# Kernel optimization log

Hardware: AMD Instinct MI355X
Metric: run time of the kernel (lower is better)

The kernel has to match this reference:

```python
import math
import jax, jax.numpy as jnp
import numpy as np

B, S, D, H = 2, 2048, 2048, 16
HD = D // H
SCALE = 1.0 / math.sqrt(HD)


def setup_inputs() -> dict:
    key = jax.random.key(0)
    kx, kq, kk, kv, ko = jax.random.split(key, 5)
    w_std = 1.0 / math.sqrt(D)
    return {
        "x": jax.random.normal(kx, (B, S, D), jnp.float32),
        "Wq": jax.random.normal(kq, (D, D), jnp.float32) * w_std,
        "Wk": jax.random.normal(kk, (D, D), jnp.float32) * w_std,
        "Wv": jax.random.normal(kv, (D, D), jnp.float32) * w_std,
        "Wo": jax.random.normal(ko, (D, D), jnp.float32) * w_std,
        "attention_mask": jnp.ones((B, S), jnp.int32),
        "sliding_window": 512,
        "sink_tokens": 4,
    }


def reference(x, Wq, Wk, Wv, Wo, attention_mask, sliding_window, sink_tokens):
    b, s, d = x.shape
    # nn.Linear(bias=False): y = x @ W^T
    q = (x @ Wq.T).reshape(b, s, H, HD).transpose(0, 2, 1, 3)  # [b,h,s,hd]
    k = (x @ Wk.T).reshape(b, s, H, HD).transpose(0, 2, 1, 3)
    v = (x @ Wv.T).reshape(b, s, H, HD).transpose(0, 2, 1, 3)

    scores = jnp.einsum("bhqd,bhkd->bhqk", q, k) * SCALE  # [b,h,s,s]

    i = jnp.arange(s)[:, None]
    j = jnp.arange(s)[None, :]
    causal = j <= i
    window = (j >= i - sliding_window + 1) & (j <= i)
    # sink mask in the source fills [0:i+1] for every row (rows < sink_tokens
    # and rows >= sink_tokens alike), i.e. it is identical to the causal mask.
    sink = causal
    allowed = causal & window & sink  # [s,s]
    pad = (attention_mask != 0)[:, None, None, :]  # [b,1,1,s]
    scores = jnp.where(allowed[None, None] & pad, scores, -jnp.inf)

    attn = jax.nn.softmax(scores, axis=-1)
    out = jnp.einsum("bhqk,bhkd->bhqd", attn, v)  # [b,h,s,hd]
    out = out.transpose(0, 2, 1, 3).reshape(b, s, d)
    return out @ Wo.T
```

## Files before the change

kernel.cpp:

```cpp
#include <hip/hip_runtime.h>
#include <stdint.h>


typedef __attribute__((ext_vector_type(8))) short short8;
typedef __attribute__((ext_vector_type(4))) float f32x4;

#define DEV static __device__ __forceinline__

DEV unsigned short f2bf(float f) {
  unsigned u = __builtin_bit_cast(unsigned, f);
  u += 0x7fffu + ((u >> 16) & 1u);
  return (unsigned short)(u >> 16);
}

DEV void async16(const void* g, void* l) {
  __builtin_amdgcn_global_load_lds(
      (const __attribute__((address_space(1))) unsigned int*)g,
      (__attribute__((address_space(3))) unsigned int*)l, 16, 0, 0);
}

__global__ __launch_bounds__(256) void cast_all(
    const float* __restrict__ x, const float* __restrict__ Wq,
    const float* __restrict__ Wk, const float* __restrict__ Wv,
    const float* __restrict__ Wo, unsigned short* __restrict__ xb,
    unsigned short* __restrict__ wqkv, unsigned short* __restrict__ wob) {
  const int bid = blockIdx.x;
  const float* src;
  unsigned short* dst;
  int i;
  if (bid < 4096) {
    src = x; dst = xb; i = bid * 256 + threadIdx.x;
  } else if (bid < 6144) {
    src = Wq; dst = wqkv; i = (bid - 4096) * 256 + threadIdx.x;
  } else if (bid < 8192) {
    src = Wk; dst = wqkv + 4194304; i = (bid - 6144) * 256 + threadIdx.x;
  } else if (bid < 10240) {
    src = Wv; dst = wqkv + 8388608; i = (bid - 8192) * 256 + threadIdx.x;
  } else {
    src = Wo; dst = wob; i = (bid - 10240) * 256 + threadIdx.x;
  }
  const float4* s4 = (const float4*)src;
  float4 a = s4[2 * (size_t)i], b = s4[2 * (size_t)i + 1];
  short8 o;
  o[0] = (short)f2bf(a.x); o[1] = (short)f2bf(a.y);
  o[2] = (short)f2bf(a.z); o[3] = (short)f2bf(a.w);
  o[4] = (short)f2bf(b.x); o[5] = (short)f2bf(b.y);
  o[6] = (short)f2bf(b.z); o[7] = (short)f2bf(b.w);
  *(short8*)(dst + 8 * (size_t)i) = o;
}

constexpr int GK = 2048, GN = 2048;

#define MFMA_BF16 __builtin_amdgcn_mfma_f32_16x16x32_bf16

#define STAGE_A(buf, h, kt)                                                  \
  {                                                                          \
    const unsigned short* g_ = Ag + (size_t)((h) * 128) * GK + (kt) * 64;    \
    char* d_ = (char*)As[buf] + (h) * 16384 + loff;                          \
    async16(g_, d_);                                                         \
    async16(g_ + (size_t)64 * GK, d_ + 8192);                                \
  }
#define STAGE_B(buf, h, kt)                                                  \
  {                                                                          \
    const unsigned short* g_ = Bg + (size_t)((h) * 128) * GK + (kt) * 64;    \
    char* d_ = (char*)Bs[buf] + (h) * 16384 + loff;                          \
    async16(g_, d_);                                                         \
    async16(g_ + (size_t)64 * GK, d_ + 8192);                                \
  }

#define READ_AF(dst, buf, mq, kc)                                            \
  _Pragma("unroll") for (int mi = 0; mi < 4; ++mi) dst[mi] =                 \
      *(const short8*)(As[buf] + aoffk[kc] + (mq)*4096 + mi * 1024);
#define READ_BF(dst, buf, kc)                                                \
  _Pragma("unroll") for (int ni = 0; ni < 4; ++ni) dst[ni] =                 \
      *(const short8*)(Bs[buf] + boffk[kc] + ni * 1024);

#define MFMA16(mq, A_, B_)                                                   \
  _Pragma("unroll") for (int mi = 0; mi < 4; ++mi)                           \
      _Pragma("unroll") for (int ni = 0; ni < 4; ++ni)                       \
      acc[(mq)*4 + mi][ni] =                                                 \
      MFMA_BF16(A_[mi], B_[ni], acc[(mq)*4 + mi][ni], 0, 0, 0);

#define MEMF __asm__ __volatile__("" ::: "memory");
#define BARR { MEMF __builtin_amdgcn_s_barrier(); MEMF }
#define SP1 __builtin_amdgcn_s_setprio(1);
#define SP0 __builtin_amdgcn_s_setprio(0);
#define LGKM0 __asm__ __volatile__("s_waitcnt lgkmcnt(0)" ::: "memory");
#define VM(n) __asm__ __volatile__("s_waitcnt vmcnt(" #n ")" ::: "memory");

template <bool STORE_BF16>
__global__ __launch_bounds__(512, 2) void gemm256(
    const unsigned short* __restrict__ A, const unsigned short* __restrict__ B,
    void* __restrict__ Cout, size_t obuf_stride) {
  __shared__ short As[2][16384];
  __shared__ short Bs[2][16384];

  const int t = threadIdx.x;
  const int lane = t & 63;
  const int quad = lane >> 4, l15 = lane & 15, l7 = l15 & 7;
  const int w = t >> 6, wm = w >> 2, wn = w & 3;

  const int nwg = (int)gridDim.x;
  const int cpx = nwg >> 3;
  const int swz = ((int)blockIdx.x & 7) * cpx + ((int)blockIdx.x >> 3);
  const int bx = swz & 15, by = swz >> 4;
  const int row0 = bx * 256, col0g = by * 256;
  const int nb = col0g >> 11, col0 = col0g & 2047;

  const int rsub = t >> 3;
  const int cg8 = ((t & 7) ^ (rsub & 7)) << 3;
  const unsigned short* Ag = A + (size_t)(row0 + rsub) * GK + cg8;
  const unsigned short* Bg = B + (size_t)(col0g + rsub) * GK + cg8;
  const int loff = rsub * 128 + (t & 7) * 16;

  int aoffk[2], boffk[2];
#pragma unroll
  for (int kc = 0; kc < 2; ++kc) {
    int swzc = (((kc * 4 + quad) ^ l7) << 3);
    aoffk[kc] = wm * 8192 + l15 * 64 + swzc;
    boffk[kc] = wn * 4096 + l15 * 64 + swzc;
  }

  f32x4 acc[8][4] = {};
  short8 afA[4], afB[4], b0[4], b1[4];

  STAGE_A(0, 0, 0) STAGE_A(0, 1, 0)
  STAGE_B(0, 0, 0) STAGE_B(0, 1, 0)
  STAGE_B(1, 0, 1) STAGE_B(1, 1, 1)
  VM(4)
  BARR
  READ_AF(afA, 0, 0, 0) READ_BF(b0, 0, 0)
  LGKM0

#pragma unroll 1
  for (int i = 0; i < 15; ++i) {
    const int t1 = 2 * i + 1;
    STAGE_A(1, 0, t1)
    BARR
    SP1 READ_AF(afB, 0, 0, 1) READ_BF(b1, 0, 1) MFMA16(0, afA, b0) SP0 LGKM0
    STAGE_A(1, 1, t1)
    BARR
    SP1 READ_AF(afA, 0, 1, 0) MFMA16(0, afB, b1) SP0 LGKM0
    STAGE_B(0, 0, t1 + 1)
    BARR
    SP1 READ_AF(afB, 0, 1, 1) MFMA16(1, afA, b0) SP0 LGKM0
    STAGE_B(0, 1, t1 + 1)
    VM(4)
    BARR
    SP1 READ_AF(afA, 1, 0, 0) READ_BF(b0, 1, 0) MFMA16(1, afB, b1) SP0 LGKM0
    STAGE_A(0, 0, t1 + 1)
    BARR
    SP1 READ_AF(afB, 1, 0, 1) READ_BF(b1, 1, 1) MFMA16(0, afA, b0) SP0 LGKM0
    STAGE_A(0, 1, t1 + 1)
    BARR
    SP1 READ_AF(afA, 1, 1, 0) MFMA16(0, afB, b1) SP0 LGKM0
    STAGE_B(1, 0, t1 + 2)
    BARR
    SP1 READ_AF(afB, 1, 1, 1) MFMA16(1, afA, b0) SP0 LGKM0
    STAGE_B(1, 1, t1 + 2)
    VM(4)
    BARR
    SP1 READ_AF(afA, 0, 0, 0) READ_BF(b0, 0, 0) MFMA16(1, afB, b1) SP0 LGKM0
  }

  {
    STAGE_A(1, 0, 31)
    BARR
    SP1 READ_AF(afB, 0, 0, 1) READ_BF(b1, 0, 1) MFMA16(0, afA, b0) SP0 LGKM0
    STAGE_A(1, 1, 31)
    BARR
    SP1 READ_AF(afA, 0, 1, 0) MFMA16(0, afB, b1) SP0 LGKM0
    BARR
    SP1 READ_AF(afB, 0, 1, 1) MFMA16(1, afA, b0) SP0 LGKM0
    VM(0)
    BARR
    SP1 READ_AF(afA, 1, 0, 0) READ_BF(b0, 1, 0) MFMA16(1, afB, b1) SP0 LGKM0
    BARR
    SP1 READ_AF(afB, 1, 0, 1) READ_BF(b1, 1, 1) MFMA16(0, afA, b0) SP0 LGKM0
    BARR
    SP1 READ_AF(afA, 1, 1, 0) MFMA16(0, afB, b1) SP0 LGKM0
    BARR
    SP1 READ_AF(afB, 1, 1, 1) MFMA16(1, afA, b0) SP0 LGKM0
    BARR
    SP1 MFMA16(1, afB, b1) SP0
  }

#pragma unroll
  for (int MI = 0; MI < 8; ++MI)
#pragma unroll
    for (int ni = 0; ni < 4; ++ni)
#pragma unroll
      for (int r = 0; r < 4; ++r) {
        int row = row0 + wm * 128 + MI * 16 + quad * 4 + r;
        int col = col0 + wn * 64 + ni * 16 + l15;
        if (STORE_BF16)
          ((unsigned short*)Cout)[nb * obuf_stride + (size_t)row * GN + col] =
              f2bf(acc[MI][ni][r]);
        else
          ((float*)Cout)[nb * obuf_stride + (size_t)row * GN + col] =
              acc[MI][ni][r];
      }
}

__global__ __launch_bounds__(256) void transpose_v(
    const unsigned short* __restrict__ vb, unsigned short* __restrict__ vtb) {
  __shared__ unsigned short tile[64][72];
  const int s0 = blockIdx.x * 64, d0 = blockIdx.y * 64, b = blockIdx.z;
  const int tid = threadIdx.x;
  const int c8 = tid & 7;
#pragma unroll
  for (int i = 0; i < 2; ++i) {
    int row = i * 32 + (tid >> 3);
    uint4 v = *(const uint4*)(vb + (size_t)(b * 2048 + s0 + row) * 2048 + d0 + c8 * 8);
    *(uint4*)&tile[row][c8 * 8] = v;
  }
  __syncthreads();
#pragma unroll
  for (int i = 0; i < 2; ++i) {
    int dr = i * 32 + (tid >> 3);
    short8 sv;
#pragma unroll
    for (int j = 0; j < 8; ++j) sv[j] = (short)tile[c8 * 8 + j][dr];
    int d = d0 + dr;
    int h = d >> 7, hd = d & 127;
    *(short8*)(vtb + ((size_t)(b * 16 + h) * 128 + hd) * 2048 + s0 + c8 * 8) = sv;
  }
}

__global__ __launch_bounds__(256, 3) void attn_mfma(
    const unsigned short* __restrict__ Qm, const unsigned short* __restrict__ Km,
    const unsigned short* __restrict__ Vt, unsigned short* __restrict__ Om,
    const int* __restrict__ amask, const int* __restrict__ winp) {
  constexpr int S = 2048, D = 2048, HD = 128;
  const float SCALE = 0.08838834764831845f;

  __shared__ short Ks[64 * 128];
  __shared__ short Vts[128 * 64];
  __shared__ short Ps[4][16 * 64];

  const int t = threadIdx.x, w = t >> 6, lane = t & 63;
  const int quad = lane >> 4, l15 = lane & 15;
  const int l7 = l15 & 7;
  const int f = blockIdx.x;
  const int qt = f >> 5, g = f & 31;
  const int h = g & 15, b = g >> 4;
  const int qi0 = qt * 64;
  const int win = winp[0];

  short8 qf[4];
  {
    const unsigned short* qp =
        Qm + (size_t)(b * S + qi0 + w * 16 + l15) * D + h * HD + quad * 8;
#pragma unroll
    for (int kc = 0; kc < 4; ++kc) qf[kc] = *(const short8*)(qp + kc * 32);
  }

  f32x4 o[8] = {};
  float m_r[4], l_r[4];
#pragma unroll
  for (int r = 0; r < 4; ++r) { m_r[r] = -1e30f; l_r[r] = 0.f; }

  int lowj = qi0 - win + 1;
  if (lowj < 0) lowj = 0;
  const int jt0 = lowj >> 6;

  const int krow = lane >> 4, kpos = lane & 15;
  const int vrow = lane >> 3, vpos = lane & 7;

  for (int jt = jt0; jt <= qt; ++jt) {
    const int j0 = jt * 64;
    __syncthreads();
#pragma unroll
    for (int ii = 0; ii < 4; ++ii) {
      int row = ii * 16 + w * 4 + krow;
      int c = kpos ^ (row & 7);
      async16(Km + (size_t)(b * S + j0 + row) * D + h * HD + c * 8,
              (char*)Ks + (ii * 16 + w * 4) * 256);
    }
#pragma unroll
    for (int ii = 0; ii < 4; ++ii) {
      int row = ii * 32 + w * 8 + vrow;
      int c = vpos ^ (row & 7);
      async16(Vt + ((size_t)(b * 16 + h) * 128 + row) * S + j0 + c * 8,
              (char*)Vts + (ii * 32 + w * 8) * 128);
    }
    __syncthreads();

    f32x4 sS[4];
#pragma unroll
    for (int ni = 0; ni < 4; ++ni) {
      f32x4 acc = {0.f, 0.f, 0.f, 0.f};
#pragma unroll
      for (int kc = 0; kc < 4; ++kc) {
        int pos = (kc * 4 + quad) ^ l7;
        short8 bk = *(const short8*)&Ks[(ni * 16 + l15) * 128 + pos * 8];
        acc = __builtin_amdgcn_mfma_f32_16x16x32_bf16(qf[kc], bk, acc, 0, 0, 0);
      }
      sS[ni] = acc;
    }

    float sv[4][4];
    int amv[4];
#pragma unroll
    for (int ni = 0; ni < 4; ++ni) amv[ni] = amask[b * S + j0 + ni * 16 + l15];
#pragma unroll
    for (int ni = 0; ni < 4; ++ni)
#pragma unroll
      for (int r = 0; r < 4; ++r) {
        int gi = qi0 + w * 16 + quad * 4 + r;
        int gj = j0 + ni * 16 + l15;
        bool ok = (gj <= gi) && (gj >= gi - win + 1) && (amv[ni] != 0);
        sv[ni][r] = ok ? sS[ni][r] * SCALE : -1e30f;
      }
    float alpha[4], mnew[4];
#pragma unroll
    for (int r = 0; r < 4; ++r) {
      float mx = fmaxf(fmaxf(sv[0][r], sv[1][r]), fmaxf(sv[2][r], sv[3][r]));
      mx = fmaxf(mx, __shfl_xor(mx, 1));
      mx = fmaxf(mx, __shfl_xor(mx, 2));
      mx = fmaxf(mx, __shfl_xor(mx, 4));
      mx = fmaxf(mx, __shfl_xor(mx, 8));
      float mn = fmaxf(m_r[r], mx);
      alpha[r] = __expf(m_r[r] - mn);
      m_r[r] = mn;
      mnew[r] = mn;
    }
    float rs[4] = {0.f, 0.f, 0.f, 0.f};
#pragma unroll
    for (int ni = 0; ni < 4; ++ni)
#pragma unroll
      for (int r = 0; r < 4; ++r) {
        float p = (sv[ni][r] > -1e29f) ? __expf(sv[ni][r] - mnew[r]) : 0.f;
        sv[ni][r] = p;
        rs[r] += p;
      }
#pragma unroll
    for (int r = 0; r < 4; ++r) {
      float s = rs[r];
      s += __shfl_xor(s, 1);
      s += __shfl_xor(s, 2);
      s += __shfl_xor(s, 4);
      s += __shfl_xor(s, 8);
      l_r[r] = l_r[r] * alpha[r] + s;
    }
#pragma unroll
    for (int ni = 0; ni < 4; ++ni)
#pragma unroll
      for (int r = 0; r < 4; ++r) {
        int row = quad * 4 + r;
        int col = ni * 16 + l15;
        int pos = (col >> 3) ^ (row & 7);
        Ps[w][row * 64 + pos * 8 + (col & 7)] = (short)f2bf(sv[ni][r]);
      }
#pragma unroll
    for (int ni2 = 0; ni2 < 8; ++ni2)
#pragma unroll
      for (int r = 0; r < 4; ++r) o[ni2][r] *= alpha[r];

    __asm__ __volatile__("s_waitcnt lgkmcnt(0)" ::: "memory");

    short8 aP[2];
#pragma unroll
    for (int kc2 = 0; kc2 < 2; ++kc2) {
      int pos = (kc2 * 4 + quad) ^ l7;
      aP[kc2] = *(const short8*)&Ps[w][l15 * 64 + pos * 8];
    }
#pragma unroll
    for (int ni2 = 0; ni2 < 8; ++ni2) {
#pragma unroll
      for (int kc2 = 0; kc2 < 2; ++kc2) {
        int pos = (kc2 * 4 + quad) ^ l7;
        short8 bv = *(const short8*)&Vts[(ni2 * 16 + l15) * 64 + pos * 8];
        o[ni2] = __builtin_amdgcn_mfma_f32_16x16x32_bf16(aP[kc2], bv, o[ni2], 0, 0, 0);
      }
    }
  }

  float inv[4];
#pragma unroll
  for (int r = 0; r < 4; ++r) inv[r] = 1.f / l_r[r];
#pragma unroll
  for (int ni2 = 0; ni2 < 8; ++ni2)
#pragma unroll
    for (int r = 0; r < 4; ++r) {
      int row = qi0 + w * 16 + quad * 4 + r;
      Om[(size_t)(b * S + row) * D + h * HD + ni2 * 16 + l15] =
          f2bf(o[ni2][r] * inv[r]);
    }
}

extern "C" void kernel_launch(void* const* d_in, const int* in_sizes, int n_in,
                              void* d_out, int out_size, void* d_ws,
                              size_t ws_size, hipStream_t stream) {
  (void)in_sizes; (void)n_in; (void)out_size; (void)ws_size;
  const float* x  = (const float*)d_in[0];
  const float* Wq = (const float*)d_in[1];
  const float* Wk = (const float*)d_in[2];
  const float* Wv = (const float*)d_in[3];
  const float* Wo = (const float*)d_in[4];
  const int* am   = (const int*)d_in[5];
  const int* win  = (const int*)d_in[6];

  char* ws = (char*)d_ws;
  unsigned short* xb   = (unsigned short*)(ws + 0);
  unsigned short* vtb  = (unsigned short*)(ws + 0);
  unsigned short* wqkv = (unsigned short*)(ws + 16777216);
  unsigned short* wob  = (unsigned short*)(ws + 41943040);
  unsigned short* qb   = (unsigned short*)(ws + 50331648);
  unsigned short* kb   = (unsigned short*)(ws + 67108864);
  unsigned short* vb   = (unsigned short*)(ws + 83886080);
  unsigned short* ab   = (unsigned short*)(ws + 100663296);

  cast_all<<<dim3(12288), dim3(256), 0, stream>>>(x, Wq, Wk, Wv, Wo, xb, wqkv, wob);

  gemm256<true><<<dim3(384), dim3(512), 0, stream>>>(xb, wqkv, qb, 8388608);

  transpose_v<<<dim3(32, 32, 2), dim3(256), 0, stream>>>(vb, vtb);

  attn_mfma<<<dim3(1024), dim3(256), 0, stream>>>(qb, kb, vtb, ab, am, win);

  gemm256<false><<<dim3(128), dim3(512), 0, stream>>>(ab, wob, d_out, 0);
}
```

Before: 370.0 us.

## Use smaller-tile GEMM for output projection and move LDS waits after barriers

The output projection switches from the 256-tile, 512-thread GEMM (128 blocks) to a new simple 128x128-tile GEMM with 256 threads (512 blocks), giving more workgroups to fill the CUs on this smaller N=2048 problem. In the big GEMM, the LDS-count waits move from the end of each stage to right after the barrier, changing where the ds_read latency is exposed. The new kernel is single-buffered with two syncthreads per 32-wide K step and no prefetch, so it may lose efficiency per block.

```diff
diff --git a/kernel.cpp b/kernel.cpp
--- a/kernel.cpp
+++ b/kernel.cpp
@@ -130,58 +130,57 @@
   VM(4)
   BARR
   READ_AF(afA, 0, 0, 0) READ_BF(b0, 0, 0)
-  LGKM0
 
 #pragma unroll 1
   for (int i = 0; i < 15; ++i) {
     const int t1 = 2 * i + 1;
     STAGE_A(1, 0, t1)
-    BARR
-    SP1 READ_AF(afB, 0, 0, 1) READ_BF(b1, 0, 1) MFMA16(0, afA, b0) SP0 LGKM0
+    BARR LGKM0
+    SP1 READ_AF(afB, 0, 0, 1) READ_BF(b1, 0, 1) MFMA16(0, afA, b0) SP0
     STAGE_A(1, 1, t1)
-    BARR
-    SP1 READ_AF(afA, 0, 1, 0) MFMA16(0, afB, b1) SP0 LGKM0
+    BARR LGKM0
+    SP1 READ_AF(afA, 0, 1, 0) MFMA16(0, afB, b1) SP0
     STAGE_B(0, 0, t1 + 1)
-    BARR
-    SP1 READ_AF(afB, 0, 1, 1) MFMA16(1, afA, b0) SP0 LGKM0
+    BARR LGKM0
+    SP1 READ_AF(afB, 0, 1, 1) MFMA16(1, afA, b0) SP0
     STAGE_B(0, 1, t1 + 1)
     VM(4)
-    BARR
-    SP1 READ_AF(afA, 1, 0, 0) READ_BF(b0, 1, 0) MFMA16(1, afB, b1) SP0 LGKM0
+    BARR LGKM0
+    SP1 READ_AF(afA, 1, 0, 0) READ_BF(b0, 1, 0) MFMA16(1, afB, b1) SP0
     STAGE_A(0, 0, t1 + 1)
-    BARR
-    SP1 READ_AF(afB, 1, 0, 1) READ_BF(b1, 1, 1) MFMA16(0, afA, b0) SP0 LGKM0
+    BARR LGKM0
+    SP1 READ_AF(afB, 1, 0, 1) READ_BF(b1, 1, 1) MFMA16(0, afA, b0) SP0
     STAGE_A(0, 1, t1 + 1)
-    BARR
-    SP1 READ_AF(afA, 1, 1, 0) MFMA16(0, afB, b1) SP0 LGKM0
+    BARR LGKM0
+    SP1 READ_AF(afA, 1, 1, 0) MFMA16(0, afB, b1) SP0
     STAGE_B(1, 0, t1 + 2)
-    BARR
-    SP1 READ_AF(afB, 1, 1, 1) MFMA16(1, afA, b0) SP0 LGKM0
+    BARR LGKM0
+    SP1 READ_AF(afB, 1, 1, 1) MFMA16(1, afA, b0) SP0
     STAGE_B(1, 1, t1 + 2)
     VM(4)
-    BARR
-    SP1 READ_AF(afA, 0, 0, 0) READ_BF(b0, 0, 0) MFMA16(1, afB, b1) SP0 LGKM0
+    BARR LGKM0
+    SP1 READ_AF(afA, 0, 0, 0) READ_BF(b0, 0, 0) MFMA16(1, afB, b1) SP0
   }
 
   {
     STAGE_A(1, 0, 31)
-    BARR
-    SP1 READ_AF(afB, 0, 0, 1) READ_BF(b1, 0, 1) MFMA16(0, afA, b0) SP0 LGKM0
+    BARR LGKM0
+    SP1 READ_AF(afB, 0, 0, 1) READ_BF(b1, 0, 1) MFMA16(0, afA, b0) SP0
     STAGE_A(1, 1, 31)
-    BARR
-    SP1 READ_AF(afA, 0, 1, 0) MFMA16(0, afB, b1) SP0 LGKM0
-    BARR
-    SP1 READ_AF(afB, 0, 1, 1) MFMA16(1, afA, b0) SP0 LGKM0
+    BARR LGKM0
+    SP1 READ_AF(afA, 0, 1, 0) MFMA16(0, afB, b1) SP0
+    BARR LGKM0
+    SP1 READ_AF(afB, 0, 1, 1) MFMA16(1, afA, b0) SP0
     VM(0)
-    BARR
-    SP1 READ_AF(afA, 1, 0, 0) READ_BF(b0, 1, 0) MFMA16(1, afB, b1) SP0 LGKM0
-    BARR
-    SP1 READ_AF(afB, 1, 0, 1) READ_BF(b1, 1, 1) MFMA16(0, afA, b0) SP0 LGKM0
-    BARR
-    SP1 READ_AF(afA, 1, 1, 0) MFMA16(0, afB, b1) SP0 LGKM0
-    BARR
-    SP1 READ_AF(afB, 1, 1, 1) MFMA16(1, afA, b0) SP0 LGKM0
-    BARR
+    BARR LGKM0
+    SP1 READ_AF(afA, 1, 0, 0) READ_BF(b0, 1, 0) MFMA16(1, afB, b1) SP0
+    BARR LGKM0
+    SP1 READ_AF(afB, 1, 0, 1) READ_BF(b1, 1, 1) MFMA16(0, afA, b0) SP0
+    BARR LGKM0
+    SP1 READ_AF(afA, 1, 1, 0) MFMA16(0, afB, b1) SP0
+    BARR LGKM0
+    SP1 READ_AF(afB, 1, 1, 1) MFMA16(1, afA, b0) SP0
+    BARR LGKM0
     SP1 MFMA16(1, afB, b1) SP0
   }
 
@@ -199,6 +198,78 @@
         else
           ((float*)Cout)[nb * obuf_stride + (size_t)row * GN + col] =
               acc[MI][ni][r];
+      }
+}
+
+template <bool STORE_BF16>
+__global__ __launch_bounds__(256) void gemm_bt(
+    const unsigned short* __restrict__ A, const unsigned short* __restrict__ B,
+    void* __restrict__ Cout, size_t obuf_stride) {
+  __shared__ short Asm[128 * 32];
+  __shared__ short Bsm[128 * 32];
+  const int t = threadIdx.x;
+  const int wave = t >> 6, lane = t & 63;
+  const int row0 = blockIdx.x * 128;
+  const int col0g = blockIdx.y * 128;
+  const int nb = col0g >> 11, col0 = col0g & 2047;
+  const int wrow = (wave >> 1) * 64, wcol = (wave & 1) * 64;
+
+  f32x4 acc[4][4] = {};
+
+  const int srow = wave * 16 + (lane >> 2);
+  const int cg = (lane & 3) ^ (lane >> 4);
+  const unsigned short* Ag0 = A + (size_t)(row0 + srow) * GK + cg * 8;
+  const unsigned short* Ag1 = A + (size_t)(row0 + 64 + srow) * GK + cg * 8;
+  const unsigned short* Bg0 = B + (size_t)(col0g + srow) * GK + cg * 8;
+  const unsigned short* Bg1 = B + (size_t)(col0g + 64 + srow) * GK + cg * 8;
+  char* lA0 = (char*)Asm + wave * 1024;
+  char* lA1 = (char*)Asm + 4096 + wave * 1024;
+  char* lB0 = (char*)Bsm + wave * 1024;
+  char* lB1 = (char*)Bsm + 4096 + wave * 1024;
+
+  const int quad = lane >> 4, l15 = lane & 15;
+  const int cpos = quad ^ ((l15 >> 2) & 3);
+  const short* ap[4];
+  const short* bp[4];
+#pragma unroll
+  for (int i = 0; i < 4; ++i) {
+    ap[i] = Asm + (wrow + i * 16 + l15) * 32 + cpos * 8;
+    bp[i] = Bsm + (wcol + i * 16 + l15) * 32 + cpos * 8;
+  }
+
+  for (int kk = 0; kk < GK; kk += 32) {
+    async16(Ag0 + kk, lA0);
+    async16(Ag1 + kk, lA1);
+    async16(Bg0 + kk, lB0);
+    async16(Bg1 + kk, lB1);
+    __syncthreads();
+    short8 af[4], bf[4];
+#pragma unroll
+    for (int i = 0; i < 4; ++i) af[i] = *(const short8*)ap[i];
+#pragma unroll
+    for (int i = 0; i < 4; ++i) bf[i] = *(const short8*)bp[i];
+#pragma unroll
+    for (int mi = 0; mi < 4; ++mi)
+#pragma unroll
+      for (int ni = 0; ni < 4; ++ni)
+        acc[mi][ni] = MFMA_BF16(af[mi], bf[ni], acc[mi][ni], 0, 0, 0);
+    __syncthreads();
+  }
+
+#pragma unroll
+  for (int mi = 0; mi < 4; ++mi)
+#pragma unroll
+    for (int ni = 0; ni < 4; ++ni)
+#pragma unroll
+      for (int r = 0; r < 4; ++r) {
+        int row = row0 + wrow + mi * 16 + quad * 4 + r;
+        int col = col0 + wcol + ni * 16 + l15;
+        if (STORE_BF16)
+          ((unsigned short*)Cout)[nb * obuf_stride + (size_t)row * GN + col] =
+              f2bf(acc[mi][ni][r]);
+        else
+          ((float*)Cout)[nb * obuf_stride + (size_t)row * GN + col] =
+              acc[mi][ni][r];
       }
 }
 
@@ -419,5 +490,5 @@
 
   attn_mfma<<<dim3(1024), dim3(256), 0, stream>>>(qb, kb, vtb, ab, am, win);
 
-  gemm256<false><<<dim3(128), dim3(512), 0, stream>>>(ab, wob, d_out, 0);
-}
+  gemm_bt<false><<<dim3(32, 16), dim3(256), 0, stream>>>(ab, wob, d_out, 0);
+}
```

Measured after the change: 372.4 us. About the same (+0.6%).
